# Kernel tuning notes

Hardware: AMD Instinct MI355X
Metric: run time of the kernel (lower is better)

The kernel has to match this reference:

```python
import jax, jax.numpy as jnp
import numpy as np

B, N, C = 4, 4096, 512
H = 8          # num_heads
M = 64         # num_landmarks
HD = C // H    # head_dim = 64
N_ITER = 6     # Newton-Schulz iterations (Nystromformer default)


def iterative_inv(mat):
    # mat: [B, H, M, M]; Nystromformer pseudo-inverse via Newton-Schulz.
    I = jnp.eye(mat.shape[-1], dtype=mat.dtype)
    K = mat
    # global-max initialization (original Nystromformer 'original' init)
    V = K.swapaxes(-1, -2) / (jnp.max(jnp.sum(K, axis=-2)) * jnp.max(jnp.sum(K, axis=-1)))
    for _ in range(N_ITER):
        KV = jnp.matmul(K, V)
        V = 0.25 * jnp.matmul(V, 13.0 * I - jnp.matmul(KV, 15.0 * I - jnp.matmul(KV, 7.0 * I - KV)))
    return V


def setup_inputs() -> dict:
    key = jax.random.key(0)
    k1, k2, k3, k4 = jax.random.split(key, 4)
    s = C ** -0.5
    return {
        "x": jax.random.normal(k1, (B, N, C), dtype=jnp.float32),
        "qkv_w": jax.random.normal(k2, (3 * C, C), dtype=jnp.float32) * s,
        "proj_w": jax.random.normal(k3, (C, C), dtype=jnp.float32) * s,
        "proj_b": jax.random.normal(k4, (C,), dtype=jnp.float32) * 0.01,
        "epoch": 1,
    }


def reference(x, qkv_w, proj_w, proj_b, epoch):
    b, n, c = x.shape
    hd = c // H
    qkv = (x @ qkv_w.T).reshape(b, n, 3, H, hd).transpose(2, 0, 3, 1, 4)  # [3,B,H,N,hd]
    Q, K, V = qkv[0], qkv[1], qkv[2]
    scale = 1.0 / np.sqrt(np.sqrt(hd)).astype(np.float32)
    Q = Q * scale
    K = K * scale
    # landmark pooling: mean over segments of length N // M
    Ql = Q.reshape(b, H, M, n // M, hd).mean(axis=-2)  # [B,H,M,hd]
    Kl = K.reshape(b, H, M, n // M, hd).mean(axis=-2)
    kernel_1 = jax.nn.softmax(jnp.einsum('bhnd,bhmd->bhnm', Q, Kl), axis=-1)   # [B,H,N,M]
    kernel_2 = jax.nn.softmax(jnp.einsum('bhmd,bhld->bhml', Ql, Kl), axis=-1)  # [B,H,M,M]
    kernel_3 = jax.nn.softmax(jnp.einsum('bhmd,bhnd->bhmn', Ql, K), axis=-1)   # [B,H,M,N]
    X = jnp.matmul(jnp.matmul(kernel_1, iterative_inv(kernel_2)), jnp.matmul(kernel_3, V))
    X = X.transpose(0, 2, 1, 3).reshape(b, n, c)
    return X @ proj_w.T + proj_b
```

## Files before the change

kernel.cpp:

```cpp
#include <hip/hip_runtime.h>
#include <hip/hip_bf16.h>
#include <stdint.h>

#define QSZe 8388608ull

typedef __attribute__((ext_vector_type(8))) short bf16x8;
typedef __attribute__((ext_vector_type(4))) float f32x4;
typedef const __attribute__((address_space(1))) unsigned int* gas1_t;
typedef __attribute__((address_space(3))) unsigned int* las3_t;

__device__ __forceinline__ float bf2f(unsigned short u) {
  return __uint_as_float(((unsigned int)u) << 16);
}
__device__ __forceinline__ unsigned short f2bf(float f) {
  unsigned int u = __float_as_uint(f);
  unsigned int r = (u + 0x7FFFu + ((u >> 16) & 1u)) >> 16;
  return (unsigned short)r;
}
__device__ __forceinline__ void gload_lds16(const void* g, void* l) {
  __builtin_amdgcn_global_load_lds((gas1_t)g, (las3_t)l, 16, 0, 0);
}
__device__ __forceinline__ unsigned int detect_f32(
    const unsigned short* __restrict__ raw_x) {
  int lane = threadIdx.x & 63;
  int big = 0;
#pragma unroll
  for (int i = 0; i < 4; i++) {
    int e = (raw_x[lane * 4 + i] >> 7) & 0xFF;
    big |= (e >= 0x8F) ? 1 : 0;
  }
  return (__ballot(big) != 0ull) ? 1u : 0u;
}

__global__ __launch_bounds__(256) void conv_all(
    const void* __restrict__ rx, const void* __restrict__ rwq,
    const void* __restrict__ rwp, unsigned short* __restrict__ cx,
    unsigned short* __restrict__ cwq, unsigned short* __restrict__ cwp,
    unsigned int* __restrict__ gstat) {
  int gid = blockIdx.x * 256 + threadIdx.x;
  if (gid == 0) {
    gstat[0] = 0u;
    gstat[1] = 0u;
  }
  unsigned int f = detect_f32((const unsigned short*)rx);
  const void* src;
  unsigned short* dst;
  int i8;
  if (gid < 1048576) {
    src = rx; dst = cx; i8 = gid * 8;
  } else if (gid < 1146880) {
    src = rwq; dst = cwq; i8 = (gid - 1048576) * 8;
  } else {
    src = rwp; dst = cwp; i8 = (gid - 1146880) * 8;
  }
  if (f) {
    const float* fp = (const float*)src;
    float4 a = *(const float4*)(fp + i8);
    float4 b = *(const float4*)(fp + i8 + 4);
    unsigned short o[8] = {f2bf(a.x), f2bf(a.y), f2bf(a.z), f2bf(a.w),
                           f2bf(b.x), f2bf(b.y), f2bf(b.z), f2bf(b.w)};
    *(uint4*)(dst + i8) = *(const uint4*)o;
  } else {
    *(uint4*)(dst + i8) = *(const uint4*)((const unsigned short*)src + i8);
  }
}

__device__ __forceinline__ void mmB(const unsigned short* A_R,
                                    const unsigned short* B_T,
                                    unsigned short* out_R,
                                    unsigned short* out_T, int wave, int lane,
                                    float s, float dg, float a7,
                                    const unsigned short* Aelt) {
  const int fr = lane & 15, fq = lane >> 4;
  bf16x8 af0 = *(const bf16x8*)&A_R[(wave * 16 + fr) * 64 + fq * 8];
  bf16x8 af1 = *(const bf16x8*)&A_R[(wave * 16 + fr) * 64 + 32 + fq * 8];
  f32x4 acc[4] = {};
#pragma unroll
  for (int j = 0; j < 4; j++) {
    bf16x8 b0 = *(const bf16x8*)&B_T[(j * 16 + fr) * 64 + fq * 8];
    bf16x8 b1 = *(const bf16x8*)&B_T[(j * 16 + fr) * 64 + 32 + fq * 8];
    acc[j] = __builtin_amdgcn_mfma_f32_16x16x32_bf16(af0, b0, acc[j], 0, 0, 0);
    acc[j] = __builtin_amdgcn_mfma_f32_16x16x32_bf16(af1, b1, acc[j], 0, 0, 0);
  }
  float ael[4][4];
  if (Aelt) {
#pragma unroll
    for (int j = 0; j < 4; j++)
#pragma unroll
      for (int r = 0; r < 4; r++)
        ael[j][r] = bf2f(Aelt[(wave * 16 + fq * 4 + r) * 64 + j * 16 + fr]);
  }
#pragma unroll
  for (int j = 0; j < 4; j++) {
    int col = j * 16 + fr;
    unsigned short pack[4];
#pragma unroll
    for (int r = 0; r < 4; r++) {
      int row = wave * 16 + fq * 4 + r;
      float v = s * acc[j][r] + ((row == col) ? dg : 0.0f);
      if (Aelt) v += a7 * ael[j][r];
      unsigned short bv = f2bf(v);
      if (out_R) out_R[row * 64 + col] = bv;
      pack[r] = bv;
    }
    if (out_T)
      *(uint2*)&out_T[col * 64 + wave * 16 + fq * 4] = *(const uint2*)pack;
  }
}

__global__ __launch_bounds__(512) void qkv_gemm_mfma(
    const unsigned short* __restrict__ w, const unsigned short* __restrict__ x,
    unsigned short* __restrict__ qkv, float* __restrict__ Ql,
    float* __restrict__ Kl, unsigned short* __restrict__ Qlb,
    unsigned short* __restrict__ Klb) {
  __shared__ __align__(16) unsigned short At[128 * 64];
  __shared__ __align__(16) unsigned short Bt[256 * 64];
  const int t = threadIdx.x;
  const int lane = t & 63, wave = t >> 6;
  const int wf = wave >> 2, wt = wave & 3;
  const int lin = blockIdx.x + blockIdx.y * 12;
  const int swz = (lin & 7) * 96 + (lin >> 3);
  const int f0 = (swz % 12) * 128, n0g = (swz / 12) * 256;
  const int srow = lane >> 3, skc = ((lane & 7) ^ srow) * 8;
  const int fr = lane & 15, fq = lane >> 4;
  const int rsw = fr & 7;
  f32x4 acc[4][4] = {};

  for (int k0 = 0; k0 < 512; k0 += 64) {
#pragma unroll
    for (int s = 0; s < 2; s++) {
      int inst = wave * 2 + s;
      int row = inst * 8 + srow;
      gload_lds16(w + (size_t)(f0 + row) * 512 + k0 + skc, &At[inst * 512]);
    }
#pragma unroll
    for (int s = 0; s < 4; s++) {
      int inst = wave * 4 + s;
      int row = inst * 8 + srow;
      gload_lds16(x + (size_t)(n0g + row) * 512 + k0 + skc, &Bt[inst * 512]);
    }
    __syncthreads();
#pragma unroll
    for (int kk = 0; kk < 64; kk += 32) {
      const int swo = (((kk >> 3) + fq) ^ rsw) << 3;
      bf16x8 af[4], bxf[4];
#pragma unroll
      for (int i = 0; i < 4; i++)
        af[i] = *(const bf16x8*)&At[(wf * 64 + i * 16 + fr) * 64 + swo];
#pragma unroll
      for (int j = 0; j < 4; j++)
        bxf[j] = *(const bf16x8*)&Bt[(wt * 64 + j * 16 + fr) * 64 + swo];
#pragma unroll
      for (int i = 0; i < 4; i++)
#pragma unroll
        for (int j = 0; j < 4; j++)
          acc[i][j] = __builtin_amdgcn_mfma_f32_16x16x32_bf16(
              af[i], bxf[j], acc[i][j], 0, 0, 0);
    }
    __syncthreads();
  }
  const int fbase = f0 + wf * 64;
  const int which = fbase >> 9;
  const int h = (fbase >> 6) & 7;
  const float scale = (which < 2) ? 0.3535533905932738f : 1.0f;
  const int b_ = n0g >> 12;
  const int bh = b_ * 8 + h;
  const int m_loc = ((n0g + wt * 64) & 4095) >> 6;
#pragma unroll
  for (int i = 0; i < 4; i++) {
    int d0 = i * 16 + fq * 4;
#pragma unroll
    for (int j = 0; j < 4; j++) {
      int nn = (n0g + wt * 64 + j * 16 + fr) & 4095;
      unsigned short pack[4];
#pragma unroll
      for (int r = 0; r < 4; r++) pack[r] = f2bf(acc[i][j][r] * scale);
      *(uint2*)&qkv[(size_t)which * QSZe + ((size_t)bh * 4096 + nn) * 64 +
                    d0] = *(const uint2*)pack;
    }
  }
  if (which < 2) {
    const float ps = scale * (1.0f / 64.0f);
#pragma unroll
    for (int i = 0; i < 4; i++) {
      float sm[4];
#pragma unroll
      for (int r = 0; r < 4; r++)
        sm[r] = acc[i][0][r] + acc[i][1][r] + acc[i][2][r] + acc[i][3][r];
#pragma unroll
      for (int mask = 1; mask < 16; mask <<= 1)
#pragma unroll
        for (int r = 0; r < 4; r++) sm[r] += __shfl_xor(sm[r], mask, 64);
      if (fr == 0) {
        int d0 = i * 16 + fq * 4;
        float4 v4 = make_float4(sm[0] * ps, sm[1] * ps, sm[2] * ps, sm[3] * ps);
        unsigned short pk[4] = {f2bf(v4.x), f2bf(v4.y), f2bf(v4.z), f2bf(v4.w)};
        size_t off = (size_t)bh * 4096 + m_loc * 64 + d0;
        if (which == 0) {
          *(float4*)&Ql[off] = v4;
          *(uint2*)&Qlb[off] = *(const uint2*)pk;
        } else {
          *(float4*)&Kl[off] = v4;
          *(uint2*)&Klb[off] = *(const uint2*)pk;
        }
      }
    }
  }
}

__global__ __launch_bounds__(256) void k2_kernel(
    const float* __restrict__ Ql, const float* __restrict__ Kl,
    float* __restrict__ k2, unsigned int* __restrict__ gstat) {
  __shared__ float KlT[64 * 64];
  __shared__ float Ps[64][65];
  int t = threadIdx.x;
  int lane = t & 63, wv = t >> 6;
  int bh = blockIdx.x;
#pragma unroll
  for (int i = 0; i < 16; i++) {
    int idx = i * 256 + t;
    KlT[(idx & 63) * 64 + (idx >> 6)] = Kl[bh * 4096 + idx];
  }
  __syncthreads();
  for (int r = wv * 16; r < wv * 16 + 16; r++) {
    float qv = Ql[(bh * 64 + r) * 64 + lane];
    float acc = 0.f;
#pragma unroll
    for (int k = 0; k < 64; k++) acc += __shfl(qv, k, 64) * KlT[k * 64 + lane];
    float mx = acc;
#pragma unroll
    for (int o = 32; o > 0; o >>= 1) mx = fmaxf(mx, __shfl_xor(mx, o, 64));
    float e = __expf(acc - mx);
    float s = e;
#pragma unroll
    for (int o = 32; o > 0; o >>= 1) s += __shfl_xor(s, o, 64);
    float p = e / s;
    k2[(bh * 64 + r) * 64 + lane] = p;
    Ps[r][lane] = p;
  }
  __syncthreads();
  float val = 0.f;
  if (t < 64) {
    for (int r = 0; r < 64; r++) val += Ps[r][t];
  } else if (t < 128) {
    int r = t - 64;
    for (int c = 0; c < 64; c++) val += Ps[r][c];
  }
  float mv = val;
#pragma unroll
  for (int o = 32; o > 0; o >>= 1) mv = fmaxf(mv, __shfl_xor(mv, o, 64));
  if (t == 0) atomicMax(gstat + 0, __float_as_uint(mv));
  if (t == 64) atomicMax(gstat + 1, __float_as_uint(mv));
}

__global__ __launch_bounds__(256) void k3_mfma(
    const unsigned short* __restrict__ Qlb,
    const unsigned short* __restrict__ qkv, float* __restrict__ Wp,
    float* __restrict__ sp) {
  __shared__ __align__(16) unsigned short Et[64 * 136];
  __shared__ __align__(16) unsigned short Vt[64 * 136];
  __shared__ float scol_l[4][64];
  const int t = threadIdx.x;
  const int lane = t & 63, wave = t >> 6;
  const int fr = lane & 15, fq = lane >> 4;
  const int slab = blockIdx.x, bh = blockIdx.y;
  const int n_base = slab * 512;
  const unsigned short* Kb = qkv + QSZe + (size_t)bh * 262144;
  const unsigned short* Vb = qkv + 2 * QSZe + (size_t)bh * 262144;
  const unsigned short* Qlp = Qlb + bh * 4096;

  bf16x8 qb[2][4];
#pragma unroll
  for (int h = 0; h < 2; h++)
#pragma unroll
    for (int j = 0; j < 4; j++)
      qb[h][j] = *(const bf16x8*)(Qlp + (j * 16 + fr) * 64 + h * 32 + fq * 8);

  f32x4 accW[4] = {};
  float scol[4] = {0.f, 0.f, 0.f, 0.f};

  for (int sc = 0; sc < 4; sc++) {
    const int n0 = n_base + sc * 128;
    {
      int n = t & 127, dg = t >> 7;
#pragma unroll
      for (int i = 0; i < 4; i++) {
        int d0 = (dg + 2 * i) * 8;
        uint4 v = *(const uint4*)(Vb + (size_t)(n0 + n) * 64 + d0);
        const unsigned short* s = (const unsigned short*)&v;
#pragma unroll
        for (int u = 0; u < 8; u++) Vt[(d0 + u) * 136 + n] = s[u];
      }
    }
    f32x4 acc[2][4] = {};
#pragma unroll
    for (int i = 0; i < 2; i++) {
      const unsigned short* Kr =
          Kb + (size_t)(n0 + wave * 32 + i * 16 + fr) * 64;
      bf16x8 a0 = *(const bf16x8*)(Kr + fq * 8);
      bf16x8 a1 = *(const bf16x8*)(Kr + 32 + fq * 8);
#pragma unroll
      for (int j = 0; j < 4; j++) {
        acc[i][j] = __builtin_amdgcn_mfma_f32_16x16x32_bf16(a0, qb[0][j],
                                                            acc[i][j], 0, 0, 0);
        acc[i][j] = __builtin_amdgcn_mfma_f32_16x16x32_bf16(a1, qb[1][j],
                                                            acc[i][j], 0, 0, 0);
      }
    }
#pragma unroll
    for (int i = 0; i < 2; i++)
#pragma unroll
      for (int j = 0; j < 4; j++) {
        unsigned short pack[4];
        float s4 = 0.f;
#pragma unroll
        for (int r = 0; r < 4; r++) {
          float e = __expf(acc[i][j][r]);
          s4 += e;
          pack[r] = f2bf(e);
        }
        scol[j] += s4;
        *(uint2*)&Et[(j * 16 + fr) * 136 + wave * 32 + i * 16 + fq * 4] =
            *(const uint2*)pack;
      }
    __syncthreads();
#pragma unroll
    for (int kk = 0; kk < 128; kk += 32) {
      bf16x8 ap = *(const bf16x8*)&Et[(wave * 16 + fr) * 136 + kk + fq * 8];
#pragma unroll
      for (int j = 0; j < 4; j++) {
        bf16x8 bv = *(const bf16x8*)&Vt[(j * 16 + fr) * 136 + kk + fq * 8];
        accW[j] =
            __builtin_amdgcn_mfma_f32_16x16x32_bf16(ap, bv, accW[j], 0, 0, 0);
      }
    }
    __syncthreads();
  }
#pragma unroll
  for (int j = 0; j < 4; j++) {
    float s = scol[j];
    s += __shfl_xor(s, 16, 64);
    s += __shfl_xor(s, 32, 64);
    if (fq == 0) scol_l[wave][j * 16 + fr] = s;
  }
  __syncthreads();
  if (t < 64)
    sp[(bh * 8 + slab) * 64 + t] =
        scol_l[0][t] + scol_l[1][t] + scol_l[2][t] + scol_l[3][t];
  float* wpo = Wp + ((size_t)bh * 8 + slab) * 4096;
#pragma unroll
  for (int j = 0; j < 4; j++)
#pragma unroll
    for (int r = 0; r < 4; r++)
      wpo[(wave * 16 + fq * 4 + r) * 64 + j * 16 + fr] = accW[j][r];
}

__global__ __launch_bounds__(256) void ns_kernel(
    const float* __restrict__ k2g, const unsigned int* __restrict__ gstat,
    const float* __restrict__ Wp, const float* __restrict__ sp,
    unsigned short* __restrict__ Ztb) {
  __shared__ __align__(16) unsigned short L[8 * 4096];
  __shared__ float ssum[64];
  unsigned short* K2R = L;
  unsigned short* VR = L + 4096;
  unsigned short* VT = L + 2 * 4096;
  unsigned short* AR = L + 3 * 4096;
  unsigned short* AT = L + 4 * 4096;
  unsigned short* T2T = L + 5 * 4096;
  unsigned short* T3T = L + 6 * 4096;
  unsigned short* WT = L + 7 * 4096;
  const int t = threadIdx.x, bh = blockIdx.x;
  const int lane = t & 63, wave = t >> 6;
  const float scale =
      1.0f / (__uint_as_float(gstat[0]) * __uint_as_float(gstat[1]));
  const float* k2p = k2g + bh * 4096;
  if (t < 64) {
    float s = 0.f;
#pragma unroll
    for (int c = 0; c < 8; c++) s += sp[(bh * 8 + c) * 64 + t];
    ssum[t] = s;
  }
  __syncthreads();
#pragma unroll
  for (int i = 0; i < 16; i++) {
    int idx = i * 256 + t;
    int m = idx >> 6, d = idx & 63;
    float kv = k2p[idx];
    K2R[idx] = f2bf(kv);
    VT[idx] = f2bf(kv * scale);
    VR[idx] = f2bf(k2p[d * 64 + m] * scale);
    float wv = 0.f;
#pragma unroll
    for (int cc = 0; cc < 8; cc++)
      wv += Wp[((size_t)(bh * 8 + cc)) * 4096 + idx];
    WT[d * 64 + m] = f2bf(wv / ssum[m]);
  }
  __syncthreads();
  for (int it = 0; it < 6; it++) {
    mmB(K2R, VT, AR, AT, wave, lane, 1.0f, 0.0f, 0.0f, nullptr);
    __syncthreads();
    mmB(AR, AT, nullptr, T2T, wave, lane, 1.0f, 15.0f, -7.0f, AR);
    __syncthreads();
    mmB(AR, T2T, nullptr, T3T, wave, lane, -1.0f, 13.0f, 0.0f, nullptr);
    __syncthreads();
    mmB(VR, T3T, VR, VT, wave, lane, 0.25f, 0.0f, 0.0f, nullptr);
    __syncthreads();
  }
  {
    const int fr = lane & 15, fq = lane >> 4;
    bf16x8 af0 = *(const bf16x8*)&WT[(wave * 16 + fr) * 64 + fq * 8];
    bf16x8 af1 = *(const bf16x8*)&WT[(wave * 16 + fr) * 64 + 32 + fq * 8];
    f32x4 acc[4] = {};
#pragma unroll
    for (int j = 0; j < 4; j++) {
      bf16x8 b0 = *(const bf16x8*)&VR[(j * 16 + fr) * 64 + fq * 8];
      bf16x8 b1 = *(const bf16x8*)&VR[(j * 16 + fr) * 64 + 32 + fq * 8];
      acc[j] =
          __builtin_amdgcn_mfma_f32_16x16x32_bf16(af0, b0, acc[j], 0, 0, 0);
      acc[j] =
          __builtin_amdgcn_mfma_f32_16x16x32_bf16(af1, b1, acc[j], 0, 0, 0);
    }
#pragma unroll
    for (int j = 0; j < 4; j++) {
      int m = j * 16 + fr;
#pragma unroll
      for (int r = 0; r < 4; r++) {
        int d = wave * 16 + fq * 4 + r;
        Ztb[bh * 4096 + d * 64 + m] = f2bf(acc[j][r]);
      }
    }
  }
}

__global__ __launch_bounds__(256) void k1x_mfma(
    const unsigned short* __restrict__ qkv,
    const unsigned short* __restrict__ Klb,
    const unsigned short* __restrict__ Ztb, unsigned short* __restrict__ X) {
  __shared__ __align__(16) unsigned short Qt[128 * 64];
  __shared__ __align__(16) unsigned short Ps[128 * 72];
  const int t = threadIdx.x;
  const int lane = t & 63, wave = t >> 6;
  const int fr = lane & 15, fq = lane >> 4;
  const int rsw = fr & 7;
  const int bh = blockIdx.x;
  const int n0 = blockIdx.y * 128;
  const unsigned short* Qb = qkv + (size_t)bh * 262144 + (size_t)n0 * 64;
  const unsigned short* Klp = Klb + bh * 4096;
  const unsigned short* Ztp = Ztb + bh * 4096;

  {
    const int srow = lane >> 3, skc = ((lane & 7) ^ srow) * 8;
#pragma unroll
    for (int s = 0; s < 4; s++) {
      int inst = wave * 4 + s;
      gload_lds16(Qb + (size_t)(inst * 8 + srow) * 64 + skc, &Qt[inst * 512]);
    }
  }
  __syncthreads();

  f32x4 acc[2][4] = {};
#pragma unroll
  for (int kk = 0; kk < 64; kk += 32) {
    bf16x8 af[2], bg[4];
#pragma unroll
    for (int i = 0; i < 2; i++)
      af[i] = *(const bf16x8*)&Qt[(wave * 32 + i * 16 + fr) * 64 +
                                  ((((kk >> 3) + fq) ^ rsw) << 3)];
#pragma unroll
    for (int j = 0; j < 4; j++)
      bg[j] = *(const bf16x8*)(Klp + (j * 16 + fr) * 64 + kk + fq * 8);
#pragma unroll
    for (int i = 0; i < 2; i++)
#pragma unroll
      for (int j = 0; j < 4; j++)
        acc[i][j] = __builtin_amdgcn_mfma_f32_16x16x32_bf16(af[i], bg[j],
                                                            acc[i][j], 0, 0, 0);
  }

#pragma unroll
  for (int i = 0; i < 2; i++) {
    float sr[4] = {0.f, 0.f, 0.f, 0.f};
#pragma unroll
    for (int j = 0; j < 4; j++)
#pragma unroll
      for (int r = 0; r < 4; r++) {
        float e = __expf(acc[i][j][r]);
        acc[i][j][r] = e;
        sr[r] += e;
      }
#pragma unroll
    for (int mask = 1; mask < 16; mask <<= 1)
#pragma unroll
      for (int r = 0; r < 4; r++) sr[r] += __shfl_xor(sr[r], mask, 64);
    float is[4];
#pragma unroll
    for (int r = 0; r < 4; r++) is[r] = 1.0f / sr[r];
#pragma unroll
    for (int j = 0; j < 4; j++)
#pragma unroll
      for (int r = 0; r < 4; r++)
        Ps[(wave * 32 + i * 16 + fq * 4 + r) * 72 + j * 16 + fr] =
            f2bf(acc[i][j][r] * is[r]);
  }
  __syncthreads();

  f32x4 ax[2][4] = {};
#pragma unroll
  for (int kk = 0; kk < 64; kk += 32) {
    bf16x8 ap[2], bz[4];
#pragma unroll
    for (int i = 0; i < 2; i++)
      ap[i] =
          *(const bf16x8*)&Ps[(wave * 32 + i * 16 + fr) * 72 + kk + fq * 8];
#pragma unroll
    for (int j = 0; j < 4; j++)
      bz[j] = *(const bf16x8*)(Ztp + (j * 16 + fr) * 64 + kk + fq * 8);
#pragma unroll
    for (int i = 0; i < 2; i++)
#pragma unroll
      for (int j = 0; j < 4; j++)
        ax[i][j] = __builtin_amdgcn_mfma_f32_16x16x32_bf16(ap[i], bz[j],
                                                           ax[i][j], 0, 0, 0);
  }

  const int b_ = bh >> 3, h = bh & 7;
#pragma unroll
  for (int i = 0; i < 2; i++) {
#pragma unroll
    for (int j = 0; j < 4; j++) {
      int c = h * 64 + j * 16 + fr;
#pragma unroll
      for (int r = 0; r < 4; r++) {
        int n = n0 + wave * 32 + i * 16 + fq * 4 + r;
        X[((size_t)(b_ * 4096 + n)) * 512 + c] = f2bf(ax[i][j][r]);
      }
    }
  }
}

__global__ __launch_bounds__(256) void proj_gemm_mfma(
    const unsigned short* __restrict__ X, const unsigned short* __restrict__ w,
    const unsigned short* __restrict__ raw_x, const void* __restrict__ raw_b,
    float* __restrict__ out) {
  __shared__ __align__(16) unsigned short At[128 * 64];
  __shared__ __align__(16) unsigned short Bt[128 * 64];
  const int t = threadIdx.x;
  const unsigned int f = detect_f32(raw_x);
  const int lane = t & 63, wave = t >> 6;
  const int wr = wave >> 1, wc = wave & 1;
  const int i0 = blockIdx.y * 128, j0 = blockIdx.x * 128;
  const int srow = lane >> 3;
  const int skc = ((lane & 7) ^ srow) * 8;
  const int fr = lane & 15, fq = lane >> 4;
  const int rsw = fr & 7;
  f32x4 acc[4][4] = {};

  for (int k0 = 0; k0 < 512; k0 += 64) {
#pragma unroll
    for (int s = 0; s < 4; s++) {
      int inst = wave * 4 + s;
      int row = inst * 8 + srow;
      gload_lds16(X + (size_t)(i0 + row) * 512 + k0 + skc, &At[inst * 512]);
      gload_lds16(w + (size_t)(j0 + row) * 512 + k0 + skc, &Bt[inst * 512]);
    }
    __syncthreads();
#pragma unroll
    for (int kk = 0; kk < 64; kk += 32) {
      const int swo = (((kk >> 3) + fq) ^ rsw) << 3;
      bf16x8 af[4], bg[4];
#pragma unroll
      for (int i = 0; i < 4; i++)
        af[i] = *(const bf16x8*)&At[(wr * 64 + i * 16 + fr) * 64 + swo];
#pragma unroll
      for (int j = 0; j < 4; j++)
        bg[j] = *(const bf16x8*)&Bt[(wc * 64 + j * 16 + fr) * 64 + swo];
#pragma unroll
      for (int i = 0; i < 4; i++)
#pragma unroll
        for (int j = 0; j < 4; j++)
          acc[i][j] = __builtin_amdgcn_mfma_f32_16x16x32_bf16(
              af[i], bg[j], acc[i][j], 0, 0, 0);
    }
    __syncthreads();
  }
#pragma unroll
  for (int j = 0; j < 4; j++) {
    int col = j0 + wc * 64 + j * 16 + fr;
    float bia = f ? ((const float*)raw_b)[col]
                  : bf2f(((const unsigned short*)raw_b)[col]);
#pragma unroll
    for (int i = 0; i < 4; i++) {
      int rbase = i0 + wr * 64 + i * 16 + fq * 4;
#pragma unroll
      for (int r = 0; r < 4; r++) {
        out[(size_t)(rbase + r) * 512 + col] = acc[i][j][r] + bia;
      }
    }
  }
}

extern "C" void kernel_launch(void* const* d_in, const int* in_sizes, int n_in,
                              void* d_out, int out_size, void* d_ws,
                              size_t ws_size, hipStream_t stream) {
  (void)in_sizes; (void)n_in; (void)out_size; (void)ws_size;

  char* w8 = (char*)d_ws;
  unsigned short* cx  = (unsigned short*)(w8 + 0);
  unsigned short* cwq = (unsigned short*)(w8 + 16777216);
  unsigned short* cwp = (unsigned short*)(w8 + 18350080);
  unsigned short* qkv = (unsigned short*)(w8 + 18876416);
  unsigned short* X   = (unsigned short*)(w8 + 69208064);
  float* Ql = (float*)(w8 + 85985280);
  float* Kl = (float*)(w8 + 86509568);
  float* k2 = (float*)(w8 + 87033856);
  unsigned short* Ztb = (unsigned short*)(w8 + 88082432);
  unsigned int* gstat = (unsigned int*)(w8 + 88606720);
  float* Wp = (float*)(w8 + 88608768);
  float* sp = (float*)(w8 + 92803072);
  unsigned short* Klb = (unsigned short*)(w8 + 92868608);
  unsigned short* Qlb = (unsigned short*)(w8 + 93130752);

  conv_all<<<4608, 256, 0, stream>>>(d_in[0], d_in[1], d_in[2], cx, cwq, cwp,
                                     gstat);
  qkv_gemm_mfma<<<dim3(12, 64), 512, 0, stream>>>(cwq, cx, qkv, Ql, Kl, Qlb,
                                                  Klb);
  k2_kernel<<<32, 256, 0, stream>>>(Ql, Kl, k2, gstat);
  k3_mfma<<<dim3(8, 32), 256, 0, stream>>>(Qlb, qkv, Wp, sp);
  ns_kernel<<<32, 256, 0, stream>>>(k2, gstat, Wp, sp, Ztb);
  k1x_mfma<<<dim3(32, 32), 256, 0, stream>>>(qkv, Klb, Ztb, X);
  proj_gemm_mfma<<<dim3(4, 128), 256, 0, stream>>>(
      X, cwp, (const unsigned short*)d_in[0], d_in[3], (float*)d_out);
}
```

Measured before the change: 235.3 us.

## Fuse x bf16 conversion into QKV GEMM and merge k2 into k3 kernel

The x float-to-bf16 conversion is removed from the standalone conversion kernel. The QKV GEMM now reads raw fp32 x, converts it in registers and writes it to swizzled LDS, so the 16MB bf16 copy of x is no longer written and re-read. The k2 softmax kernel becomes an extra block column (slab 8) of the k3 kernel, which removes one launch and lets the two run concurrently. The cost is that the GEMM's B operand now goes through synchronous register loads instead of async global_load_lds, which reads twice the bytes per tile and may stall the MFMA loop.

```diff
diff --git a/kernel.cpp b/kernel.cpp
--- a/kernel.cpp
+++ b/kernel.cpp
@@ -32,26 +32,23 @@
   return (__ballot(big) != 0ull) ? 1u : 0u;
 }
 
-__global__ __launch_bounds__(256) void conv_all(
-    const void* __restrict__ rx, const void* __restrict__ rwq,
-    const void* __restrict__ rwp, unsigned short* __restrict__ cx,
+__global__ __launch_bounds__(256) void conv_w(
+    const void* __restrict__ rwq, const void* __restrict__ rwp,
     unsigned short* __restrict__ cwq, unsigned short* __restrict__ cwp,
-    unsigned int* __restrict__ gstat) {
+    unsigned int* __restrict__ gstat, const unsigned short* __restrict__ rx) {
   int gid = blockIdx.x * 256 + threadIdx.x;
   if (gid == 0) {
     gstat[0] = 0u;
     gstat[1] = 0u;
   }
-  unsigned int f = detect_f32((const unsigned short*)rx);
+  unsigned int f = detect_f32(rx);
   const void* src;
   unsigned short* dst;
   int i8;
-  if (gid < 1048576) {
-    src = rx; dst = cx; i8 = gid * 8;
-  } else if (gid < 1146880) {
-    src = rwq; dst = cwq; i8 = (gid - 1048576) * 8;
+  if (gid < 98304) {
+    src = rwq; dst = cwq; i8 = gid * 8;
   } else {
-    src = rwp; dst = cwp; i8 = (gid - 1146880) * 8;
+    src = rwp; dst = cwp; i8 = (gid - 98304) * 8;
   }
   if (f) {
     const float* fp = (const float*)src;
@@ -109,7 +106,7 @@
 }
 
 __global__ __launch_bounds__(512) void qkv_gemm_mfma(
-    const unsigned short* __restrict__ w, const unsigned short* __restrict__ x,
+    const unsigned short* __restrict__ w, const void* __restrict__ xraw,
     unsigned short* __restrict__ qkv, float* __restrict__ Ql,
     float* __restrict__ Kl, unsigned short* __restrict__ Qlb,
     unsigned short* __restrict__ Klb) {
@@ -118,10 +115,12 @@
   const int t = threadIdx.x;
   const int lane = t & 63, wave = t >> 6;
   const int wf = wave >> 2, wt = wave & 3;
+  const unsigned int isf = detect_f32((const unsigned short*)xraw);
   const int lin = blockIdx.x + blockIdx.y * 12;
   const int swz = (lin & 7) * 96 + (lin >> 3);
   const int f0 = (swz % 12) * 128, n0g = (swz / 12) * 256;
-  const int srow = lane >> 3, skc = ((lane & 7) ^ srow) * 8;
+  const int srow = lane >> 3, z = lane & 7;
+  const int skc = (z ^ srow) * 8;
   const int fr = lane & 15, fq = lane >> 4;
   const int rsw = fr & 7;
   f32x4 acc[4][4] = {};
@@ -133,11 +132,27 @@
       int row = inst * 8 + srow;
       gload_lds16(w + (size_t)(f0 + row) * 512 + k0 + skc, &At[inst * 512]);
     }
-#pragma unroll
-    for (int s = 0; s < 4; s++) {
-      int inst = wave * 4 + s;
-      int row = inst * 8 + srow;
-      gload_lds16(x + (size_t)(n0g + row) * 512 + k0 + skc, &Bt[inst * 512]);
+    if (!isf) {
+      const unsigned short* xb = (const unsigned short*)xraw;
+#pragma unroll
+      for (int s = 0; s < 4; s++) {
+        int inst = wave * 4 + s;
+        int row = inst * 8 + srow;
+        gload_lds16(xb + (size_t)(n0g + row) * 512 + k0 + skc,
+                    &Bt[inst * 512]);
+      }
+    } else {
+      const float* xf = (const float*)xraw;
+#pragma unroll
+      for (int s = 0; s < 4; s++) {
+        int row = (wave * 4 + s) * 8 + srow;
+        const float* src = xf + (size_t)(n0g + row) * 512 + k0 + z * 8;
+        float4 a = *(const float4*)src;
+        float4 b = *(const float4*)(src + 4);
+        unsigned short o[8] = {f2bf(a.x), f2bf(a.y), f2bf(a.z), f2bf(a.w),
+                               f2bf(b.x), f2bf(b.y), f2bf(b.z), f2bf(b.w)};
+        *(uint4*)&Bt[row * 64 + skc] = *(const uint4*)o;
+      }
     }
     __syncthreads();
 #pragma unroll
@@ -208,62 +223,62 @@
   }
 }
 
-__global__ __launch_bounds__(256) void k2_kernel(
-    const float* __restrict__ Ql, const float* __restrict__ Kl,
-    float* __restrict__ k2, unsigned int* __restrict__ gstat) {
-  __shared__ float KlT[64 * 64];
-  __shared__ float Ps[64][65];
-  int t = threadIdx.x;
-  int lane = t & 63, wv = t >> 6;
-  int bh = blockIdx.x;
-#pragma unroll
-  for (int i = 0; i < 16; i++) {
-    int idx = i * 256 + t;
-    KlT[(idx & 63) * 64 + (idx >> 6)] = Kl[bh * 4096 + idx];
-  }
-  __syncthreads();
-  for (int r = wv * 16; r < wv * 16 + 16; r++) {
-    float qv = Ql[(bh * 64 + r) * 64 + lane];
-    float acc = 0.f;
-#pragma unroll
-    for (int k = 0; k < 64; k++) acc += __shfl(qv, k, 64) * KlT[k * 64 + lane];
-    float mx = acc;
-#pragma unroll
-    for (int o = 32; o > 0; o >>= 1) mx = fmaxf(mx, __shfl_xor(mx, o, 64));
-    float e = __expf(acc - mx);
-    float s = e;
-#pragma unroll
-    for (int o = 32; o > 0; o >>= 1) s += __shfl_xor(s, o, 64);
-    float p = e / s;
-    k2[(bh * 64 + r) * 64 + lane] = p;
-    Ps[r][lane] = p;
-  }
-  __syncthreads();
-  float val = 0.f;
-  if (t < 64) {
-    for (int r = 0; r < 64; r++) val += Ps[r][t];
-  } else if (t < 128) {
-    int r = t - 64;
-    for (int c = 0; c < 64; c++) val += Ps[r][c];
-  }
-  float mv = val;
-#pragma unroll
-  for (int o = 32; o > 0; o >>= 1) mv = fmaxf(mv, __shfl_xor(mv, o, 64));
-  if (t == 0) atomicMax(gstat + 0, __float_as_uint(mv));
-  if (t == 64) atomicMax(gstat + 1, __float_as_uint(mv));
-}
-
-__global__ __launch_bounds__(256) void k3_mfma(
+__global__ __launch_bounds__(256) void k3k2_mfma(
     const unsigned short* __restrict__ Qlb,
     const unsigned short* __restrict__ qkv, float* __restrict__ Wp,
-    float* __restrict__ sp) {
-  __shared__ __align__(16) unsigned short Et[64 * 136];
-  __shared__ __align__(16) unsigned short Vt[64 * 136];
-  __shared__ float scol_l[4][64];
+    float* __restrict__ sp, const float* __restrict__ Ql,
+    const float* __restrict__ Kl, float* __restrict__ k2,
+    unsigned int* __restrict__ gstat) {
+  __shared__ __align__(16) unsigned char SM[35840];
   const int t = threadIdx.x;
   const int lane = t & 63, wave = t >> 6;
+  const int slab = blockIdx.x, bh = blockIdx.y;
+
+  if (slab == 8) {
+    float* KlT = (float*)SM;
+    float* Ps = (float*)(SM + 16384);
+#pragma unroll
+    for (int i = 0; i < 16; i++) {
+      int idx = i * 256 + t;
+      KlT[(idx & 63) * 64 + (idx >> 6)] = Kl[bh * 4096 + idx];
+    }
+    __syncthreads();
+    for (int r = wave * 16; r < wave * 16 + 16; r++) {
+      float qv = Ql[(bh * 64 + r) * 64 + lane];
+      float acc = 0.f;
+#pragma unroll
+      for (int k = 0; k < 64; k++)
+        acc += __shfl(qv, k, 64) * KlT[k * 64 + lane];
+      float mx = acc;
+#pragma unroll
+      for (int o = 32; o > 0; o >>= 1) mx = fmaxf(mx, __shfl_xor(mx, o, 64));
+      float e = __expf(acc - mx);
+      float s = e;
+#pragma unroll
+      for (int o = 32; o > 0; o >>= 1) s += __shfl_xor(s, o, 64);
+      float p = e / s;
+      k2[(bh * 64 + r) * 64 + lane] = p;
+      Ps[r * 65 + lane] = p;
+    }
+    __syncthreads();
+    float val = 0.f;
+    if (t < 64) {
+      for (int r = 0; r < 64; r++) val += Ps[r * 65 + t];
+    } else if (t < 128) {
+      int r = t - 64;
+      for (int c = 0; c < 64; c++) val += Ps[r * 65 + c];
+    }
+    float mv = val;
+#pragma unroll
+    for (int o = 32; o > 0; o >>= 1) mv = fmaxf(mv, __shfl_xor(mv, o, 64));
+    if (t == 0) atomicMax(gstat + 0, __float_as_uint(mv));
+    if (t == 64) atomicMax(gstat + 1, __float_as_uint(mv));
+    return;
+  }
+  unsigned short* Et = (unsigned short*)SM;
+  unsigned short* Vt = (unsigned short*)(SM + 17408);
+  float* scol_l = (float*)(SM + 34816);
   const int fr = lane & 15, fq = lane >> 4;
-  const int slab = blockIdx.x, bh = blockIdx.y;
   const int n_base = slab * 512;
   const unsigned short* Kb = qkv + QSZe + (size_t)bh * 262144;
   const unsigned short* Vb = qkv + 2 * QSZe + (size_t)bh * 262144;
@@ -341,12 +356,12 @@
     float s = scol[j];
     s += __shfl_xor(s, 16, 64);
     s += __shfl_xor(s, 32, 64);
-    if (fq == 0) scol_l[wave][j * 16 + fr] = s;
+    if (fq == 0) scol_l[wave * 64 + j * 16 + fr] = s;
   }
   __syncthreads();
   if (t < 64)
-    sp[(bh * 8 + slab) * 64 + t] =
-        scol_l[0][t] + scol_l[1][t] + scol_l[2][t] + scol_l[3][t];
+    sp[(bh * 8 + slab) * 64 + t] = scol_l[0 * 64 + t] + scol_l[1 * 64 + t] +
+                                   scol_l[2 * 64 + t] + scol_l[3 * 64 + t];
   float* wpo = Wp + ((size_t)bh * 8 + slab) * 4096;
 #pragma unroll
   for (int j = 0; j < 4; j++)
@@ -605,7 +620,6 @@
   (void)in_sizes; (void)n_in; (void)out_size; (void)ws_size;
 
   char* w8 = (char*)d_ws;
-  unsigned short* cx  = (unsigned short*)(w8 + 0);
   unsigned short* cwq = (unsigned short*)(w8 + 16777216);
   unsigned short* cwp = (unsigned short*)(w8 + 18350080);
   unsigned short* qkv = (unsigned short*)(w8 + 18876416);
@@ -620,12 +634,12 @@
   unsigned short* Klb = (unsigned short*)(w8 + 92868608);
   unsigned short* Qlb = (unsigned short*)(w8 + 93130752);
 
-  conv_all<<<4608, 256, 0, stream>>>(d_in[0], d_in[1], d_in[2], cx, cwq, cwp,
-                                     gstat);
-  qkv_gemm_mfma<<<dim3(12, 64), 512, 0, stream>>>(cwq, cx, qkv, Ql, Kl, Qlb,
-                                                  Klb);
-  k2_kernel<<<32, 256, 0, stream>>>(Ql, Kl, k2, gstat);
-  k3_mfma<<<dim3(8, 32), 256, 0, stream>>>(Qlb, qkv, Wp, sp);
+  conv_w<<<512, 256, 0, stream>>>(d_in[1], d_in[2], cwq, cwp, gstat,
+                                  (const unsigned short*)d_in[0]);
+  qkv_gemm_mfma<<<dim3(12, 64), 512, 0, stream>>>(cwq, d_in[0], qkv, Ql, Kl,
+                                                  Qlb, Klb);
+  k3k2_mfma<<<dim3(9, 32), 256, 0, stream>>>(Qlb, qkv, Wp, sp, Ql, Kl, k2,
+                                             gstat);
   ns_kernel<<<32, 256, 0, stream>>>(k2, gstat, Wp, sp, Ztb);
   k1x_mfma<<<dim3(32, 32), 256, 0, stream>>>(qkv, Klb, Ztb, X);
   proj_gemm_mfma<<<dim3(4, 128), 256, 0, stream>>>(
```

Measured after the change: 238.3 us. No clear change (+1.3%).
